# Kernel optimization log

Measured on AMD Instinct MI355X. Metric: run time of the kernel, lower is better.

## Reference

```python
import jax, jax.numpy as jnp
import numpy as np

B, C, N = 8, 512, 2048  # batch, channels (=size), tokens


def setup_inputs() -> dict:
    key = jax.random.key(0)
    ks = jax.random.split(key, 9)
    s = 1.0 / np.sqrt(C)
    return {
        "q": jax.random.normal(ks[0], (B, C, N), dtype=jnp.float32),
        "k": jax.random.normal(ks[1], (B, C, N), dtype=jnp.float32),
        "v": jax.random.normal(ks[2], (B, C, N), dtype=jnp.float32),
        "wq": jax.random.normal(ks[3], (C, C), dtype=jnp.float32) * s,
        "bq": jax.random.normal(ks[4], (C,), dtype=jnp.float32) * s,
        "wk": jax.random.normal(ks[5], (C, C), dtype=jnp.float32) * s,
        "bk": jax.random.normal(ks[6], (C,), dtype=jnp.float32) * s,
        "wv": jax.random.normal(ks[7], (C, C), dtype=jnp.float32) * s,
        "bv": jax.random.normal(ks[8], (C,), dtype=jnp.float32) * s,
    }


def _proj(x, w, b):
    # 1x1 conv over channels: out[b,c,n] = sum_i w[c,i] x[b,i,n] + b[c]
    return jnp.einsum('ci,bin->bcn', w, x) + b[None, :, None]


def reference(q, k, v, wq, bq, wk, bk, wv, bv):
    residual = q                                   # [B, C, N]
    qp = _proj(q, wq, bq).transpose(0, 2, 1)       # [B, N, C]
    kp = _proj(k, wk, bk).transpose(0, 2, 1)       # [B, N, C]
    vp = _proj(v, wv, bv).transpose(0, 2, 1)       # [B, N, C]
    attn = jnp.einsum('bnc,bmc->bnm', qp, kp)      # raw QK^T, no scale/softmax
    out = jnp.einsum('bnm,bmc->bnc', attn, vp)     # [B, N, C]
    return out.transpose(0, 2, 1) + residual       # [B, C, N]
```

## Files before the change

### kernel.cpp

```cpp
#include <hip/hip_runtime.h>
#include <hip/hip_bf16.h>
#include <stdint.h>

#define B_ 8
#define C_ 512
#define N_ 2048

typedef __bf16 bf16_t;
typedef bf16_t bf16x8 __attribute__((ext_vector_type(8)));
typedef bf16_t bf16x4 __attribute__((ext_vector_type(4)));
typedef float f32x4 __attribute__((ext_vector_type(4)));

__global__ __launch_bounds__(256) void weights_kernel(
    const float* __restrict__ wq, const float* __restrict__ wk,
    const float* __restrict__ wv, bf16_t* __restrict__ WqT,
    bf16_t* __restrict__ Wkb, bf16_t* __restrict__ Wvb)
{
    __shared__ bf16_t tile[64][65];
    const int t = blockIdx.x;
    const int tid = threadIdx.x;
    if (t < 64) {
        const int i0 = (t & 7) * 64, c0 = (t >> 3) * 64;
        const int cx = (tid & 15) * 4, ry = tid >> 4;
#pragma unroll
        for (int r = ry; r < 64; r += 16) {
            float4 f = *(const float4*)&wq[(size_t)(c0 + r) * C_ + i0 + cx];
            tile[r][cx + 0] = (bf16_t)f.x; tile[r][cx + 1] = (bf16_t)f.y;
            tile[r][cx + 2] = (bf16_t)f.z; tile[r][cx + 3] = (bf16_t)f.w;
        }
        __syncthreads();
#pragma unroll
        for (int r = ry; r < 64; r += 16) {
            bf16x4 o;
            o[0] = tile[cx + 0][r]; o[1] = tile[cx + 1][r];
            o[2] = tile[cx + 2][r]; o[3] = tile[cx + 3][r];
            *(bf16x4*)&WqT[(size_t)(i0 + r) * C_ + c0 + cx] = o;
        }
    } else {
        int j = t - 64;
        const float* src = (j < 64) ? wk : wv;
        bf16_t* dst = (j < 64) ? Wkb : Wvb;
        j &= 63;
#pragma unroll
        for (int p = 0; p < 4; ++p) {
            const int i = j * 4096 + p * 1024 + tid * 4;
            float4 f = *(const float4*)(src + i);
            bf16x4 o;
            o[0] = (bf16_t)f.x; o[1] = (bf16_t)f.y;
            o[2] = (bf16_t)f.z; o[3] = (bf16_t)f.w;
            *(bf16x4*)(dst + i) = o;
        }
    }
}

__global__ __launch_bounds__(256) void prep_q_kernel(
    const float* __restrict__ q, bf16_t* __restrict__ qT, bf16_t* __restrict__ qc)
{
    __shared__ bf16_t tile[64][65];
    const int b = blockIdx.z;
    const float* src = q + (size_t)b * C_ * N_;
    bf16_t* dT = qT + (size_t)b * N_ * C_;
    bf16_t* dc = qc + (size_t)b * C_ * N_;
    const int n0 = blockIdx.x * 64, c0 = blockIdx.y * 64;
    const int t = threadIdx.x;
    const int cx = (t & 15) * 4, ry = t >> 4;
#pragma unroll
    for (int r = ry; r < 64; r += 16) {
        float4 f = *(const float4*)&src[(size_t)(c0 + r) * N_ + n0 + cx];
        bf16x4 o;
        o[0] = (bf16_t)f.x; o[1] = (bf16_t)f.y;
        o[2] = (bf16_t)f.z; o[3] = (bf16_t)f.w;
        tile[r][cx + 0] = o[0]; tile[r][cx + 1] = o[1];
        tile[r][cx + 2] = o[2]; tile[r][cx + 3] = o[3];
        *(bf16x4*)&dc[(size_t)(c0 + r) * N_ + n0 + cx] = o;
    }
    __syncthreads();
#pragma unroll
    for (int r = ry; r < 64; r += 16) {
        bf16x4 o;
        o[0] = tile[cx + 0][r]; o[1] = tile[cx + 1][r];
        o[2] = tile[cx + 2][r]; o[3] = tile[cx + 3][r];
        *(bf16x4*)&dT[(size_t)(n0 + r) * C_ + c0 + cx] = o;
    }
}

__global__ __launch_bounds__(256) void gemm_dkv(
    const float* __restrict__ Kin, const float* __restrict__ Vin,
    bf16_t* __restrict__ Dp, float* __restrict__ sk4, float* __restrict__ sv4)
{
    __shared__ __align__(16) float As[128 * 64];
    __shared__ __align__(16) float Bs[128 * 64];

    const int f = blockIdx.x;
    const int xcd = f & 7, sl = f >> 3;
    const int g = xcd + 8 * (sl >> 4), t5 = sl & 15;
    const int bz = g >> 2, sp = g & 3;
    const int m0 = (t5 >> 2) * 128, n0 = (t5 & 3) * 128;
    const int kbeg = sp * 512;

    const int tid = threadIdx.x, lane = tid & 63, wave = tid >> 6;
    const int wr = wave >> 1, wc = wave & 1;

    const float* Ab = Kin + (size_t)bz * C_ * N_;
    const float* Bb = Vin + (size_t)bz * C_ * N_;

    f32x4 acc[4][4];
#pragma unroll
    for (int i = 0; i < 4; ++i)
#pragma unroll
        for (int j = 0; j < 4; ++j) acc[i][j] = 0.f;

    const int prow = tid >> 4;
    const int cs   = (tid & 15) ^ (prow & 7);
    const int ldso = tid * 16;

    const int srr = tid >> 1, hh = tid & 1;
    float hsA = 0.f, hsB = 0.f;
    const bool doA = (n0 == 0), doB = (m0 == 0);

    for (int t = 0; t < 8; ++t) {
        const float* ga = Ab + (size_t)(m0 + prow) * N_ + kbeg + t * 64 + cs * 4;
        const float* gb = Bb + (size_t)(n0 + prow) * N_ + kbeg + t * 64 + cs * 4;
#pragma unroll
        for (int p = 0; p < 8; ++p)
            __builtin_amdgcn_global_load_lds(
                (const __attribute__((address_space(1))) void*)(ga + (size_t)p * 16 * N_),
                (__attribute__((address_space(3))) void*)((char*)As + ldso + p * 4096),
                16, 0, 0);
#pragma unroll
        for (int p = 0; p < 8; ++p)
            __builtin_amdgcn_global_load_lds(
                (const __attribute__((address_space(1))) void*)(gb + (size_t)p * 16 * N_),
                (__attribute__((address_space(3))) void*)((char*)Bs + ldso + p * 4096),
                16, 0, 0);
        __syncthreads();

#pragma unroll
        for (int kk = 0; kk < 64; kk += 32) {
            bf16x8 af[4], bfr[4];
            const int kcol = kk + (lane >> 4) * 8;
            const int c1 = kcol >> 2;
#pragma unroll
            for (int m = 0; m < 4; ++m) {
                const int r = wr * 64 + (lane & 15) + m * 16;
                f32x4 lo = *(const f32x4*)((const char*)As + r * 256 + ((c1 ^ (r & 7)) << 4));
                f32x4 hi = *(const f32x4*)((const char*)As + r * 256 + (((c1 + 1) ^ (r & 7)) << 4));
                bf16x8 fr;
                fr[0] = (bf16_t)lo[0]; fr[1] = (bf16_t)lo[1];
                fr[2] = (bf16_t)lo[2]; fr[3] = (bf16_t)lo[3];
                fr[4] = (bf16_t)hi[0]; fr[5] = (bf16_t)hi[1];
                fr[6] = (bf16_t)hi[2]; fr[7] = (bf16_t)hi[3];
                af[m] = fr;
            }
#pragma unroll
            for (int n = 0; n < 4; ++n) {
                const int r = wc * 64 + (lane & 15) + n * 16;
                f32x4 lo = *(const f32x4*)((const char*)Bs + r * 256 + ((c1 ^ (r & 7)) << 4));
                f32x4 hi = *(const f32x4*)((const char*)Bs + r * 256 + (((c1 + 1) ^ (r & 7)) << 4));
                bf16x8 fr;
                fr[0] = (bf16_t)lo[0]; fr[1] = (bf16_t)lo[1];
                fr[2] = (bf16_t)lo[2]; fr[3] = (bf16_t)lo[3];
                fr[4] = (bf16_t)hi[0]; fr[5] = (bf16_t)hi[1];
                fr[6] = (bf16_t)hi[2]; fr[7] = (bf16_t)hi[3];
                bfr[n] = fr;
            }
#pragma unroll
            for (int m = 0; m < 4; ++m)
#pragma unroll
                for (int n = 0; n < 4; ++n)
                    acc[m][n] = __builtin_amdgcn_mfma_f32_16x16x32_bf16(
                        af[m], bfr[n], acc[m][n], 0, 0, 0);
        }

        if (doA) {
#pragma unroll
            for (int u = 0; u < 8; ++u) {
                const int slot = ((hh * 8 + u) + srr) & 15;
                f32x4 vv = *(const f32x4*)((const char*)As + srr * 256 + slot * 16);
                hsA += vv[0] + vv[1] + vv[2] + vv[3];
            }
        }
        if (doB) {
#pragma unroll
            for (int u = 0; u < 8; ++u) {
                const int slot = ((hh * 8 + u) + srr) & 15;
                f32x4 vv = *(const f32x4*)((const char*)Bs + srr * 256 + slot * 16);
                hsB += vv[0] + vv[1] + vv[2] + vv[3];
            }
        }
        __syncthreads();
    }

    const int rj = (lane >> 4) * 4;
    const int cc = lane & 15;
    const size_t sCC = (size_t)C_ * C_;
    const int z = bz * 4 + sp;
#pragma unroll
    for (int m = 0; m < 4; ++m) {
#pragma unroll
        for (int n = 0; n < 4; ++n) {
            const int col = n0 + wc * 64 + n * 16 + cc;
            f32x4 vv = acc[m][n];
#pragma unroll
            for (int j = 0; j < 4; ++j) {
                const int row = m0 + wr * 64 + m * 16 + rj + j;
                Dp[(size_t)z * sCC + (size_t)row * C_ + col] = (bf16_t)vv[j];
            }
        }
    }
    if (doA) {
        hsA += __shfl_xor(hsA, 1, 64);
        if (!hh) sk4[(size_t)(sp * B_ + bz) * C_ + m0 + srr] = hsA;
    }
    if (doB) {
        hsB += __shfl_xor(hsB, 1, 64);
        if (!hh) sv4[(size_t)(sp * B_ + bz) * C_ + n0 + srr] = hsB;
    }
}

__global__ __launch_bounds__(256) void reduce_mv_kernel(
    const bf16_t* __restrict__ Pt, bf16_t* __restrict__ Out,
    const bf16_t* __restrict__ Wvb, const bf16_t* __restrict__ Wkb,
    const float* __restrict__ sk4, const float* __restrict__ sv4,
    float* __restrict__ u, float* __restrict__ w)
{
    __shared__ float svec[C_];
    const size_t sCC = (size_t)C_ * C_;
    const int bid = blockIdx.x, tid = threadIdx.x;
    if (bid < 1024) {
        size_t idx = ((size_t)bid * 256 + tid) * 8;
        size_t b = idx / sCC;
        size_t r = idx - b * sCC;
        const bf16_t* base = Pt + (b * 4) * sCC + r;
        float acc[8];
#pragma unroll
        for (int j = 0; j < 8; ++j) acc[j] = 0.f;
#pragma unroll
        for (int s = 0; s < 4; ++s) {
            bf16x8 pv = *(const bf16x8*)(base + (size_t)s * sCC);
#pragma unroll
            for (int j = 0; j < 8; ++j) acc[j] += (float)pv[j];
        }
        bf16x8 o;
#pragma unroll
        for (int j = 0; j < 8; ++j) o[j] = (bf16_t)acc[j];
        *(bf16x8*)(Out + idx) = o;
    } else {
        const int b2 = bid - 1024, b = b2 >> 1, sel = b2 & 1;
        const float* s4 = (sel ? sk4 : sv4) + (size_t)b * C_;
        const size_t st = (size_t)B_ * C_;
#pragma unroll
        for (int rr = 0; rr < 2; ++rr) {
            const int j = tid * 2 + rr;
            svec[j] = s4[j] + s4[st + j] + s4[2 * st + j] + s4[3 * st + j];
        }
        __syncthreads();
        const bf16_t* W = sel ? Wkb : Wvb;
        float* o = (sel ? w : u) + (size_t)b * C_;
        const int c = tid * 2;
#pragma unroll
        for (int rr = 0; rr < 2; ++rr) {
            const bf16_t* row = W + (size_t)(c + rr) * C_;
            float acc = 0.f;
            for (int j = 0; j < C_; j += 8) {
                bf16x8 vv = *(const bf16x8*)(row + j);
#pragma unroll
                for (int e = 0; e < 8; ++e) acc += (float)vv[e] * svec[j + e];
            }
            o[c + rr] = acc;
        }
    }
}

template <int EPI>
__global__ __launch_bounds__(256) void gemm64_nt(
    const bf16_t* __restrict__ A, const bf16_t* __restrict__ Bm,
    bf16_t* __restrict__ Cout, size_t sA, size_t sB, size_t sC,
    const float* __restrict__ e0, const float* __restrict__ e1,
    const float* __restrict__ e2, const float* __restrict__ e3,
    const float* __restrict__ bqv, float* __restrict__ hout)
{
    __shared__ __align__(16) bf16_t As[64 * 64];
    __shared__ __align__(16) bf16_t Bs[64 * 64];

    const int tid = threadIdx.x, lane = tid & 63, wave = tid >> 6;
    const int wr = wave >> 1, wc = wave & 1;
    const int bz = blockIdx.z;
    const int m0 = blockIdx.y * 64, n0 = blockIdx.x * 64;
    const int K = C_;

    const bf16_t* Ab = A + (size_t)bz * sA;
    const bf16_t* Bb = Bm + (size_t)bz * sB;

    f32x4 acc[2][2];
#pragma unroll
    for (int i = 0; i < 2; ++i)
#pragma unroll
        for (int j = 0; j < 2; ++j) acc[i][j] = 0.f;

    const int srow = tid >> 3;
    const int scol = ((tid & 7) ^ (srow & 7)) * 8;
    const int ldso = tid * 16;

    float hacc = 0.f;
    const bool doH = (EPI == 2) && (blockIdx.x == 0);

    for (int t = 0; t < 8; ++t) {
        const bf16_t* ga = Ab + (size_t)(m0 + srow) * K + t * 64 + scol;
        const bf16_t* gb = Bb + (size_t)(n0 + srow) * K + t * 64 + scol;
#pragma unroll
        for (int p = 0; p < 2; ++p)
            __builtin_amdgcn_global_load_lds(
                (const __attribute__((address_space(1))) void*)(ga + (size_t)p * 32 * K),
                (__attribute__((address_space(3))) void*)((char*)As + ldso + p * 4096),
                16, 0, 0);
#pragma unroll
        for (int p = 0; p < 2; ++p)
            __builtin_amdgcn_global_load_lds(
                (const __attribute__((address_space(1))) void*)(gb + (size_t)p * 32 * K),
                (__attribute__((address_space(3))) void*)((char*)Bs + ldso + p * 4096),
                16, 0, 0);
        __syncthreads();

#pragma unroll
        for (int kk = 0; kk < 64; kk += 32) {
            bf16x8 af[2], bfr[2];
            const int kcol = kk + (lane >> 4) * 8;
            const int kc = kcol >> 3;
#pragma unroll
            for (int m = 0; m < 2; ++m) {
                const int r = wr * 32 + (lane & 15) + m * 16;
                af[m] = *(const bf16x8*)((const char*)As + r * 128 +
                                         ((kc ^ (r & 7)) << 4));
            }
#pragma unroll
            for (int n = 0; n < 2; ++n) {
                const int r = wc * 32 + (lane & 15) + n * 16;
                bfr[n] = *(const bf16x8*)((const char*)Bs + r * 128 +
                                          ((kc ^ (r & 7)) << 4));
            }
#pragma unroll
            for (int m = 0; m < 2; ++m)
#pragma unroll
                for (int n = 0; n < 2; ++n)
                    acc[m][n] = __builtin_amdgcn_mfma_f32_16x16x32_bf16(
                        af[m], bfr[n], acc[m][n], 0, 0, 0);
        }
        if (doH) {
            const int rr = tid >> 2, qq = tid & 3;
#pragma unroll
            for (int u = 0; u < 2; ++u) {
                const int c = qq * 2 + u;
                bf16x8 av = *(const bf16x8*)((const char*)As + rr * 128 +
                                             ((c ^ (rr & 7)) << 4));
                const float* bp = bqv + t * 64 + c * 8;
#pragma unroll
                for (int e = 0; e < 8; ++e) hacc += (float)av[e] * bp[e];
            }
        }
        __syncthreads();
    }

    const int rj = (lane >> 4) * 4;
    const int cc = lane & 15;
#pragma unroll
    for (int m = 0; m < 2; ++m) {
#pragma unroll
        for (int n = 0; n < 2; ++n) {
            const int col = n0 + wc * 32 + n * 16 + cc;
            f32x4 vv = acc[m][n];
#pragma unroll
            for (int j = 0; j < 4; ++j) {
                const int row = m0 + wr * 32 + m * 16 + rj + j;
                float val = vv[j];
                if (EPI == 1)
                    val += e0[bz * C_ + row] * e1[col] +
                           e2[row] * (e3[bz * C_ + col] + 2048.0f * e1[col]);
                Cout[(size_t)bz * sC + (size_t)row * C_ + col] = (bf16_t)val;
            }
        }
    }
    if (doH) {
        hacc += __shfl_xor(hacc, 1, 64);
        hacc += __shfl_xor(hacc, 2, 64);
        if ((tid & 3) == 0) hout[bz * C_ + m0 + (tid >> 2)] = hacc;
    }
}

__global__ __launch_bounds__(256) void gemm_final(
    const bf16_t* __restrict__ A, const bf16_t* __restrict__ Bm,
    float* __restrict__ Cout, const bf16_t* __restrict__ qc,
    const float* __restrict__ hvec)
{
    __shared__ __align__(16) bf16_t As[128 * 64];
    __shared__ __align__(16) bf16_t Bs[128 * 64];

    const int f = blockIdx.x;
    const int xcd = f & 7, sl = f >> 3;
    const int g = xcd + 8 * (sl >> 2);
    const int m0 = (sl & 3) * 128;
    const int bz = g >> 4;
    const int n0 = (g & 15) * 128;
    const int K = C_;

    const int tid = threadIdx.x, lane = tid & 63, wave = tid >> 6;
    const int wr = wave >> 1, wc = wave & 1;

    const bf16_t* Ab = A + (size_t)bz * ((size_t)C_ * C_);
    const bf16_t* Bb = Bm + (size_t)bz * ((size_t)N_ * C_);

    f32x4 acc[4][4];
#pragma unroll
    for (int i = 0; i < 4; ++i)
#pragma unroll
        for (int j = 0; j < 4; ++j) acc[i][j] = 0.f;

    const int srow = tid >> 3;
    const int scol = ((tid & 7) ^ (srow & 7)) * 8;
    const int ldso = tid * 16;

    for (int t = 0; t < 8; ++t) {
        const bf16_t* ga = Ab + (size_t)(m0 + srow) * K + t * 64 + scol;
        const bf16_t* gb = Bb + (size_t)(n0 + srow) * K + t * 64 + scol;
#pragma unroll
        for (int p = 0; p < 4; ++p)
            __builtin_amdgcn_global_load_lds(
                (const __attribute__((address_space(1))) void*)(ga + (size_t)p * 32 * K),
                (__attribute__((address_space(3))) void*)((char*)As + ldso + p * 4096),
                16, 0, 0);
#pragma unroll
        for (int p = 0; p < 4; ++p)
            __builtin_amdgcn_global_load_lds(
                (const __attribute__((address_space(1))) void*)(gb + (size_t)p * 32 * K),
                (__attribute__((address_space(3))) void*)((char*)Bs + ldso + p * 4096),
                16, 0, 0);
        __syncthreads();

#pragma unroll
        for (int kk = 0; kk < 64; kk += 32) {
            bf16x8 af[4], bfr[4];
            const int kcol = kk + (lane >> 4) * 8;
            const int kc = kcol >> 3;
#pragma unroll
            for (int m = 0; m < 4; ++m) {
                const int r = wr * 64 + (lane & 15) + m * 16;
                af[m] = *(const bf16x8*)((const char*)As + r * 128 +
                                         ((kc ^ (r & 7)) << 4));
            }
#pragma unroll
            for (int n = 0; n < 4; ++n) {
                const int r = wc * 64 + (lane & 15) + n * 16;
                bfr[n] = *(const bf16x8*)((const char*)Bs + r * 128 +
                                          ((kc ^ (r & 7)) << 4));
            }
#pragma unroll
            for (int m = 0; m < 4; ++m)
#pragma unroll
                for (int n = 0; n < 4; ++n)
                    acc[m][n] = __builtin_amdgcn_mfma_f32_16x16x32_bf16(
                        af[m], bfr[n], acc[m][n], 0, 0, 0);
        }
        __syncthreads();
    }

    const int rj = (lane >> 4) * 4;
    const int cc = lane & 15;
    const size_t ob = (size_t)bz * ((size_t)C_ * N_);
#pragma unroll
    for (int m = 0; m < 4; ++m) {
#pragma unroll
        for (int n = 0; n < 4; ++n) {
            const int col = n0 + wc * 64 + n * 16 + cc;
            f32x4 vv = acc[m][n];
#pragma unroll
            for (int j = 0; j < 4; ++j) {
                const int row = m0 + wr * 64 + m * 16 + rj + j;
                const size_t o = ob + (size_t)row * N_ + col;
                Cout[o] = vv[j] + hvec[bz * C_ + row] + (float)qc[o];
            }
        }
    }
}

extern "C" void kernel_launch(void* const* d_in, const int* in_sizes, int n_in,
                              void* d_out, int out_size, void* d_ws, size_t ws_size,
                              hipStream_t stream)
{
    (void)in_sizes; (void)n_in; (void)out_size; (void)ws_size;
    const float* q  = (const float*)d_in[0];
    const float* k  = (const float*)d_in[1];
    const float* v  = (const float*)d_in[2];
    const float* wq = (const float*)d_in[3];
    const float* bq = (const float*)d_in[4];
    const float* wk = (const float*)d_in[5];
    const float* bk = (const float*)d_in[6];
    const float* wv = (const float*)d_in[7];
    const float* bv = (const float*)d_in[8];
    float* out = (float*)d_out;

    char* ws = (char*)d_ws;
    const size_t WSZ = (size_t)C_ * C_ * 2;
    const size_t TSZ = (size_t)B_ * N_ * C_ * 2;
    const size_t SCZ = (size_t)B_ * C_ * C_ * 2;
    const size_t VSZ = (size_t)B_ * C_ * 4;
    size_t off = 0;
    bf16_t* Wkb  = (bf16_t*)(ws + off); off += WSZ;
    bf16_t* Wvb  = (bf16_t*)(ws + off); off += WSZ;
    bf16_t* WqTb = (bf16_t*)(ws + off); off += WSZ;
    bf16_t* qT   = (bf16_t*)(ws + off); off += TSZ;
    bf16_t* qc   = (bf16_t*)(ws + off); off += TSZ;
    bf16_t* Dp   = (bf16_t*)(ws + off); off += TSZ;
    bf16_t* D    = (bf16_t*)(ws + off); off += SCZ;
    bf16_t* P1   = (bf16_t*)(ws + off); off += SCZ;
    bf16_t* St   = (bf16_t*)(ws + off); off += SCZ;
    bf16_t* HT   = (bf16_t*)(ws + off); off += SCZ;
    float*  sk4  = (float*)(ws + off);  off += 4 * VSZ;
    float*  sv4  = (float*)(ws + off);  off += 4 * VSZ;
    float*  uu   = (float*)(ws + off);  off += VSZ;
    float*  wwv  = (float*)(ws + off);  off += VSZ;
    float*  hb   = (float*)(ws + off);  off += VSZ;

    const dim3 blk(256);
    const size_t sCC = (size_t)C_ * C_;

    weights_kernel<<<dim3(192), blk, 0, stream>>>(wq, wk, wv, WqTb, Wkb, Wvb);

    prep_q_kernel<<<dim3(N_ / 64, C_ / 64, B_), blk, 0, stream>>>(q, qT, qc);

    gemm_dkv<<<dim3(512), blk, 0, stream>>>(k, v, Dp, sk4, sv4);

    reduce_mv_kernel<<<dim3(1040), blk, 0, stream>>>(
        Dp, D, Wvb, Wkb, sk4, sv4, uu, wwv);

    gemm64_nt<0><<<dim3(C_ / 64, C_ / 64, B_), blk, 0, stream>>>(
        Wvb, D, P1, 0, sCC, sCC, nullptr, nullptr, nullptr, nullptr, nullptr, nullptr);

    gemm64_nt<1><<<dim3(C_ / 64, C_ / 64, B_), blk, 0, stream>>>(
        P1, Wkb, St, sCC, 0, sCC, uu, bk, bv, wwv, nullptr, nullptr);

    gemm64_nt<2><<<dim3(C_ / 64, C_ / 64, B_), blk, 0, stream>>>(
        St, WqTb, HT, sCC, 0, sCC, nullptr, nullptr, nullptr, nullptr, bq, hb);

    gemm_final<<<dim3(512), blk, 0, stream>>>(HT, qT, out, qc, hb);
}
```

Baseline: 108.9 us.

## Precompute Wk^T·Wq product to remove one batched 512x512 GEMM

Reassociates the matrix chain so that the batch-independent product of the key and query weights (M) is computed once, instead of applying Wk and Wq as two separate batched GEMMs. The bias cross terms are recomputed as small vectors and scalars (gk, va, s1, s2) in the weights and reduce kernels and folded into the remaining GEMM's epilogue. This removes one 8-batch 512x512x512 GEMM launch and its St intermediate buffer. In exchange it adds one unbatched GEMM and some matrix-vector work, and rounding M to bf16 may change accuracy.

After: 139.8 us. 28.4% more time.

```diff
diff --git a/kernel.cpp b/kernel.cpp
--- a/kernel.cpp
+++ b/kernel.cpp
@@ -13,18 +13,26 @@
 
 __global__ __launch_bounds__(256) void weights_kernel(
     const float* __restrict__ wq, const float* __restrict__ wk,
-    const float* __restrict__ wv, bf16_t* __restrict__ WqT,
-    bf16_t* __restrict__ Wkb, bf16_t* __restrict__ Wvb)
+    const float* __restrict__ wv, const float* __restrict__ bq,
+    const float* __restrict__ bk,
+    bf16_t* __restrict__ WqT, bf16_t* __restrict__ WkT,
+    bf16_t* __restrict__ Wvb, float* __restrict__ gk,
+    float* __restrict__ va, float* __restrict__ s1p)
 {
     __shared__ bf16_t tile[64][65];
+    __shared__ float fl[512];
+    __shared__ float red[256];
     const int t = blockIdx.x;
     const int tid = threadIdx.x;
-    if (t < 64) {
-        const int i0 = (t & 7) * 64, c0 = (t >> 3) * 64;
+    if (t < 128) {
+        const float* src = (t < 64) ? wq : wk;
+        bf16_t* dst = (t < 64) ? WqT : WkT;
+        const int j = t & 63;
+        const int i0 = (j & 7) * 64, c0 = (j >> 3) * 64;
         const int cx = (tid & 15) * 4, ry = tid >> 4;
 #pragma unroll
         for (int r = ry; r < 64; r += 16) {
-            float4 f = *(const float4*)&wq[(size_t)(c0 + r) * C_ + i0 + cx];
+            float4 f = *(const float4*)&src[(size_t)(c0 + r) * C_ + i0 + cx];
             tile[r][cx + 0] = (bf16_t)f.x; tile[r][cx + 1] = (bf16_t)f.y;
             tile[r][cx + 2] = (bf16_t)f.z; tile[r][cx + 3] = (bf16_t)f.w;
         }
@@ -34,22 +42,43 @@
             bf16x4 o;
             o[0] = tile[cx + 0][r]; o[1] = tile[cx + 1][r];
             o[2] = tile[cx + 2][r]; o[3] = tile[cx + 3][r];
-            *(bf16x4*)&WqT[(size_t)(i0 + r) * C_ + c0 + cx] = o;
-        }
-    } else {
-        int j = t - 64;
-        const float* src = (j < 64) ? wk : wv;
-        bf16_t* dst = (j < 64) ? Wkb : Wvb;
-        j &= 63;
+            *(bf16x4*)&dst[(size_t)(i0 + r) * C_ + c0 + cx] = o;
+        }
+    } else if (t < 192) {
+        const int j = t - 128;
 #pragma unroll
         for (int p = 0; p < 4; ++p) {
             const int i = j * 4096 + p * 1024 + tid * 4;
-            float4 f = *(const float4*)(src + i);
+            float4 f = *(const float4*)(wv + i);
             bf16x4 o;
             o[0] = (bf16_t)f.x; o[1] = (bf16_t)f.y;
             o[2] = (bf16_t)f.z; o[3] = (bf16_t)f.w;
-            *(bf16x4*)(dst + i) = o;
-        }
+            *(bf16x4*)(Wvb + i) = o;
+        }
+    } else if (t < 194) {
+        const float* W = (t == 192) ? wk : wq;
+        const float* bb = (t == 192) ? bq : bk;
+        float* out = (t == 192) ? gk : va;
+        fl[tid] = bb[tid]; fl[tid + 256] = bb[tid + 256];
+        __syncthreads();
+        float a0 = 0.f, a1 = 0.f;
+#pragma unroll 4
+        for (int c1 = 0; c1 < C_; ++c1) {
+            float2 ww = *(const float2*)&W[(size_t)c1 * C_ + 2 * tid];
+            a0 += ww.x * fl[c1];
+            a1 += ww.y * fl[c1];
+        }
+        out[2 * tid] = a0;
+        out[2 * tid + 1] = a1;
+    } else {
+        float p = bk[tid] * bq[tid] + bk[tid + 256] * bq[tid + 256];
+        red[tid] = p;
+        __syncthreads();
+        for (int s = 128; s > 0; s >>= 1) {
+            if (tid < s) red[tid] += red[tid + s];
+            __syncthreads();
+        }
+        if (tid == 0) s1p[0] = red[0];
     }
 }
 
@@ -220,11 +249,13 @@
 
 __global__ __launch_bounds__(256) void reduce_mv_kernel(
     const bf16_t* __restrict__ Pt, bf16_t* __restrict__ Out,
-    const bf16_t* __restrict__ Wvb, const bf16_t* __restrict__ Wkb,
+    const bf16_t* __restrict__ Wvb, const bf16_t* __restrict__ M,
     const float* __restrict__ sk4, const float* __restrict__ sv4,
-    float* __restrict__ u, float* __restrict__ w)
+    const float* __restrict__ gk, const float* __restrict__ s1p,
+    float* __restrict__ u, float* __restrict__ vbraw, float* __restrict__ s2)
 {
     __shared__ float svec[C_];
+    __shared__ float red[256];
     const size_t sCC = (size_t)C_ * C_;
     const int bid = blockIdx.x, tid = threadIdx.x;
     if (bid < 1024) {
@@ -245,9 +276,9 @@
 #pragma unroll
         for (int j = 0; j < 8; ++j) o[j] = (bf16_t)acc[j];
         *(bf16x8*)(Out + idx) = o;
-    } else {
-        const int b2 = bid - 1024, b = b2 >> 1, sel = b2 & 1;
-        const float* s4 = (sel ? sk4 : sv4) + (size_t)b * C_;
+    } else if (bid < 1032) {
+        const int b = bid - 1024;
+        const float* s4 = sv4 + (size_t)b * C_;
         const size_t st = (size_t)B_ * C_;
 #pragma unroll
         for (int rr = 0; rr < 2; ++rr) {
@@ -255,20 +286,48 @@
             svec[j] = s4[j] + s4[st + j] + s4[2 * st + j] + s4[3 * st + j];
         }
         __syncthreads();
-        const bf16_t* W = sel ? Wkb : Wvb;
-        float* o = (sel ? w : u) + (size_t)b * C_;
         const int c = tid * 2;
 #pragma unroll
         for (int rr = 0; rr < 2; ++rr) {
-            const bf16_t* row = W + (size_t)(c + rr) * C_;
+            const bf16_t* row = Wvb + (size_t)(c + rr) * C_;
             float acc = 0.f;
             for (int j = 0; j < C_; j += 8) {
                 bf16x8 vv = *(const bf16x8*)(row + j);
 #pragma unroll
                 for (int e = 0; e < 8; ++e) acc += (float)vv[e] * svec[j + e];
             }
-            o[c + rr] = acc;
-        }
+            u[b * C_ + c + rr] = acc;
+        }
+    } else {
+        const int b = bid - 1032;
+        const float* s4 = sk4 + (size_t)b * C_;
+        const size_t st = (size_t)B_ * C_;
+#pragma unroll
+        for (int rr = 0; rr < 2; ++rr) {
+            const int j = tid * 2 + rr;
+            svec[j] = s4[j] + s4[st + j] + s4[2 * st + j] + s4[3 * st + j];
+        }
+        __syncthreads();
+        const int c = tid * 2;
+#pragma unroll
+        for (int rr = 0; rr < 2; ++rr) {
+            const bf16_t* row = M + (size_t)(c + rr) * C_;
+            float acc = 0.f;
+            for (int j = 0; j < C_; j += 8) {
+                bf16x8 vv = *(const bf16x8*)(row + j);
+#pragma unroll
+                for (int e = 0; e < 8; ++e) acc += (float)vv[e] * svec[j + e];
+            }
+            vbraw[b * C_ + c + rr] = acc;
+        }
+        float p = svec[tid] * gk[tid] + svec[tid + 256] * gk[tid + 256];
+        red[tid] = p;
+        __syncthreads();
+        for (int s = 128; s > 0; s >>= 1) {
+            if (tid < s) red[tid] += red[tid + s];
+            __syncthreads();
+        }
+        if (tid == 0) s2[b] = red[0] + 2048.0f * s1p[0];
     }
 }
 
@@ -278,7 +337,8 @@
     bf16_t* __restrict__ Cout, size_t sA, size_t sB, size_t sC,
     const float* __restrict__ e0, const float* __restrict__ e1,
     const float* __restrict__ e2, const float* __restrict__ e3,
-    const float* __restrict__ bqv, float* __restrict__ hout)
+    const float* __restrict__ bqv, float* __restrict__ hout,
+    const float* __restrict__ s1p, const float* __restrict__ s2p)
 {
     __shared__ __align__(16) bf16_t As[64 * 64];
     __shared__ __align__(16) bf16_t Bs[64 * 64];
@@ -303,7 +363,7 @@
     const int ldso = tid * 16;
 
     float hacc = 0.f;
-    const bool doH = (EPI == 2) && (blockIdx.x == 0);
+    const bool doH = (EPI == 3) && (blockIdx.x == 0);
 
     for (int t = 0; t < 8; ++t) {
         const bf16_t* ga = Ab + (size_t)(m0 + srow) * K + t * 64 + scol;
@@ -373,7 +433,7 @@
             for (int j = 0; j < 4; ++j) {
                 const int row = m0 + wr * 32 + m * 16 + rj + j;
                 float val = vv[j];
-                if (EPI == 1)
+                if (EPI == 3)
                     val += e0[bz * C_ + row] * e1[col] +
                            e2[row] * (e3[bz * C_ + col] + 2048.0f * e1[col]);
                 Cout[(size_t)bz * sC + (size_t)row * C_ + col] = (bf16_t)val;
@@ -383,7 +443,11 @@
     if (doH) {
         hacc += __shfl_xor(hacc, 1, 64);
         hacc += __shfl_xor(hacc, 2, 64);
-        if ((tid & 3) == 0) hout[bz * C_ + m0 + (tid >> 2)] = hacc;
+        if ((tid & 3) == 0) {
+            const int row = m0 + (tid >> 2);
+            hout[bz * C_ + row] = hacc + e0[bz * C_ + row] * s1p[0] +
+                                  e2[row] * s2p[bz];
+        }
     }
 }
 
@@ -503,43 +567,50 @@
     const size_t TSZ = (size_t)B_ * N_ * C_ * 2;
     const size_t SCZ = (size_t)B_ * C_ * C_ * 2;
     const size_t VSZ = (size_t)B_ * C_ * 4;
+    const size_t sCC = (size_t)C_ * C_;
     size_t off = 0;
-    bf16_t* Wkb  = (bf16_t*)(ws + off); off += WSZ;
+    bf16_t* WqTb = (bf16_t*)(ws + off); off += WSZ;
+    bf16_t* WkTb = (bf16_t*)(ws + off); off += WSZ;
     bf16_t* Wvb  = (bf16_t*)(ws + off); off += WSZ;
-    bf16_t* WqTb = (bf16_t*)(ws + off); off += WSZ;
+    bf16_t* M    = (bf16_t*)(ws + off); off += WSZ;
     bf16_t* qT   = (bf16_t*)(ws + off); off += TSZ;
     bf16_t* qc   = (bf16_t*)(ws + off); off += TSZ;
     bf16_t* Dp   = (bf16_t*)(ws + off); off += TSZ;
     bf16_t* D    = (bf16_t*)(ws + off); off += SCZ;
     bf16_t* P1   = (bf16_t*)(ws + off); off += SCZ;
-    bf16_t* St   = (bf16_t*)(ws + off); off += SCZ;
     bf16_t* HT   = (bf16_t*)(ws + off); off += SCZ;
     float*  sk4  = (float*)(ws + off);  off += 4 * VSZ;
     float*  sv4  = (float*)(ws + off);  off += 4 * VSZ;
+    float*  gk   = (float*)(ws + off);  off += C_ * 4;
+    float*  va   = (float*)(ws + off);  off += C_ * 4;
+    float*  s1p  = (float*)(ws + off);  off += 64;
+    float*  s2   = (float*)(ws + off);  off += 64;
     float*  uu   = (float*)(ws + off);  off += VSZ;
-    float*  wwv  = (float*)(ws + off);  off += VSZ;
+    float*  vbr  = (float*)(ws + off);  off += VSZ;
     float*  hb   = (float*)(ws + off);  off += VSZ;
 
     const dim3 blk(256);
-    const size_t sCC = (size_t)C_ * C_;
-
-    weights_kernel<<<dim3(192), blk, 0, stream>>>(wq, wk, wv, WqTb, Wkb, Wvb);
+
+    weights_kernel<<<dim3(195), blk, 0, stream>>>(
+        wq, wk, wv, bq, bk, WqTb, WkTb, Wvb, gk, va, s1p);
+
+    gemm64_nt<0><<<dim3(8, 8, 1), blk, 0, stream>>>(
+        WqTb, WkTb, M, 0, 0, 0,
+        nullptr, nullptr, nullptr, nullptr, nullptr, nullptr, nullptr, nullptr);
 
     prep_q_kernel<<<dim3(N_ / 64, C_ / 64, B_), blk, 0, stream>>>(q, qT, qc);
 
     gemm_dkv<<<dim3(512), blk, 0, stream>>>(k, v, Dp, sk4, sv4);
 
     reduce_mv_kernel<<<dim3(1040), blk, 0, stream>>>(
-        Dp, D, Wvb, Wkb, sk4, sv4, uu, wwv);
-
-    gemm64_nt<0><<<dim3(C_ / 64, C_ / 64, B_), blk, 0, stream>>>(
-        Wvb, D, P1, 0, sCC, sCC, nullptr, nullptr, nullptr, nullptr, nullptr, nullptr);
-
-    gemm64_nt<1><<<dim3(C_ / 64, C_ / 64, B_), blk, 0, stream>>>(
-        P1, Wkb, St, sCC, 0, sCC, uu, bk, bv, wwv, nullptr, nullptr);
-
-    gemm64_nt<2><<<dim3(C_ / 64, C_ / 64, B_), blk, 0, stream>>>(
-        St, WqTb, HT, sCC, 0, sCC, nullptr, nullptr, nullptr, nullptr, bq, hb);
+        Dp, D, Wvb, M, sk4, sv4, gk, s1p, uu, vbr, s2);
+
+    gemm64_nt<0><<<dim3(8, 8, B_), blk, 0, stream>>>(
+        Wvb, D, P1, 0, sCC, sCC,
+        nullptr, nullptr, nullptr, nullptr, nullptr, nullptr, nullptr, nullptr);
+
+    gemm64_nt<3><<<dim3(8, 8, B_), blk, 0, stream>>>(
+        P1, M, HT, sCC, 0, sCC, uu, va, bv, vbr, gk, hb, s1p, s2);
 
     gemm_final<<<dim3(512), blk, 0, stream>>>(HT, qT, out, qc, hb);
 }
```
